# Performance work log

Hardware: AMD Instinct MI355X
Metric: run time of the kernel (lower is better)

Reference implementation:

```python
import jax, jax.numpy as jnp
import numpy as np

I, O, R = 64, 64, 896          # input / output / regulatory protein counts
N = I + O + R                  # total GRN size
WARMUP = 25                    # warmup_count


def setup_inputs() -> dict:
    key = jax.random.key(0)
    k1, k2, k3, k4 = jax.random.split(key, 4)
    return {
        "inputs": jax.random.uniform(k1, (16384, I), dtype=jnp.float32),
        "identifiers": jax.random.uniform(k2, (N,), dtype=jnp.float32),
        "enhancers": jax.random.uniform(k3, (N,), dtype=jnp.float32),
        "inhibitors": jax.random.uniform(k4, (N,), dtype=jnp.float32),
        "beta": jnp.full((1,), 2.0, dtype=jnp.float32),
        "delta": jnp.full((1,), 1.0, dtype=jnp.float32),
    }


def _signatures(identifiers, enhancers, inhibitors, beta):
    # sig[j, i] = exp(-beta * |tag_j - id_i|): affinity of protein j regulating protein i.
    enh = jnp.exp(-beta * jnp.abs(enhancers[:, None] - identifiers[None, :]))
    inh = jnp.exp(-beta * jnp.abs(inhibitors[:, None] - identifiers[None, :]))
    # output proteins do not regulate others -> zero their rows
    mask = jnp.ones((N,), dtype=enh.dtype).at[I:I + O].set(0.0)[:, None]
    return enh * mask, inh * mask


def _step(conc, sig_diff, delta):
    # conc: [..., N]; sig_diff = enh_sigs - inh_sigs: [N, N]
    dc = (delta / N) * (conc @ sig_diff)
    new = jnp.maximum(conc + dc, 0.0)
    reg = new[..., I:]                                    # outputs + regulatory
    s = jnp.sum(reg, axis=-1, keepdims=True)
    reg = jnp.where(s > 0, reg / s, reg)                  # renormalize
    return jnp.concatenate([conc[..., :I], reg], axis=-1)  # inputs clamped


def reference(inputs, identifiers, enhancers, inhibitors, beta, delta):
    b, d = beta[0], delta[0]
    enh_s, inh_s = _signatures(identifiers, enhancers, inhibitors, b)
    sig_diff = enh_s - inh_s

    # setup(): uniform initial concentrations; warmup(): shared sequential steps
    conc0 = jnp.full((N,), 1.0 / N, dtype=jnp.float32)
    def warm(c, _):
        return _step(c, sig_diff, d), None
    conc, _ = jax.lax.scan(warm, conc0, None, length=WARMUP)

    # per-sample (batched instead of tf.map_fn): set input concs, one step
    B = inputs.shape[0]
    batch_conc = jnp.concatenate(
        [inputs, jnp.broadcast_to(conc[I:], (B, N - I))], axis=-1)
    new = _step(batch_conc, sig_diff, d)
    return new[..., I:I + O]  # output protein concentrations [B, O]
```

## Files before the change

kernel.cpp:

```cpp
#include <hip/hip_runtime.h>
#include <math.h>

#define NJ 960
#define NSRC 896
#define NWARM 25

typedef unsigned long long u64;
typedef unsigned int u32;

#define RK_O   0u
#define CT_O   896u
#define HD_O   1856u
#define WK_F   8192u
#define BASE_F (WK_F + 64u * 960u)

#define TAG_RK 0x524B0001u
#define TAG_CT 0x43540001u
#define TAG_HD 0x48440001u

__device__ __forceinline__ void ast(u64* p, u64 v) {
  __hip_atomic_store(p, v, __ATOMIC_RELAXED, __HIP_MEMORY_SCOPE_AGENT);
}
__device__ __forceinline__ u64 ald(const u64* p) {
  return __hip_atomic_load(p, __ATOMIC_RELAXED, __HIP_MEMORY_SCOPE_AGENT);
}
__device__ __forceinline__ u32 poll32(const u64* p, u32 tag) {
  u64 v = ald(p);
  while ((u32)(v >> 32) != tag) { __builtin_amdgcn_s_sleep(1); v = ald(p); }
  return (u32)v;
}

__global__ __launch_bounds__(256) void front_k(const float* __restrict__ ident,
                                               const float* __restrict__ enh,
                                               const float* __restrict__ inh,
                                               const float* __restrict__ beta,
                                               const float* __restrict__ delta,
                                               void* __restrict__ wsv) {
  u64* RK = (u64*)wsv + RK_O;
  u64* CT = (u64*)wsv + CT_O;
  u64* HD = (u64*)wsv + HD_O;
  float* Wk = (float*)wsv + WK_F;
  float* base = (float*)wsv + BASE_F;

  const int tid = threadIdx.x;
  const float bb = beta[0];
  const float dN = delta[0] / 1024.0f;

  if (blockIdx.x > 0) {
    const int g = (blockIdx.x - 1) * 256 + tid;
    const int c8 = g & 7;
    if (g < NSRC * 8) {
      int m = g >> 3;
      float myE = enh[128 + m], myI = inh[128 + m];
      int re = 0, ri = 0;
      for (int i = 112 * c8; i < 112 * c8 + 112; ++i) {
        float ev = enh[128 + i], iv = inh[128 + i];
        re += (ev < myE || (ev == myE && i < m)) ? 1 : 0;
        ri += (iv < myI || (iv == myI && i < m)) ? 1 : 0;
      }
      int p = re | (ri << 16);
      p += __shfl_xor(p, 1); p += __shfl_xor(p, 2); p += __shfl_xor(p, 4);
      if (c8 == 0) ast(&RK[m], ((u64)TAG_RK << 32) | (u32)p);
    }
    {
      int j = g >> 3;
      float cj = ident[64 + j];
      int ce = 0, ci = 0;
      for (int i = 112 * c8; i < 112 * c8 + 112; ++i) {
        ce += (enh[128 + i] <= cj) ? 1 : 0;
        ci += (inh[128 + i] <= cj) ? 1 : 0;
      }
      int p = ce | (ci << 16);
      p += __shfl_xor(p, 1); p += __shfl_xor(p, 2); p += __shfl_xor(p, 4);
      if (c8 == 0) ast(&CT[j], ((u64)TAG_CT << 32) | (u32)p);
    }
    {
      int j = g >> 3;
      float cj = ident[64 + j];
      float h = 0.0f;
      for (int k = 8 * c8; k < 8 * c8 + 8; ++k)
        h += expf(-bb * fabsf(enh[k] - cj)) - expf(-bb * fabsf(inh[k] - cj));
      h += __shfl_xor(h, 1); h += __shfl_xor(h, 2); h += __shfl_xor(h, 4);
      if (c8 == 0)
        ast(&HD[j], ((u64)TAG_HD << 32) |
                    (u64)__float_as_uint(dN * h * (1.0f / 1024.0f)));
    }
    {
      int k = g / 120;
      int jb = (g % 120) * 8;
      float ek = enh[k], ik = inh[k];
      #pragma unroll
      for (int u = 0; u < 8; ++u) {
        float cj = ident[64 + jb + u];
        Wk[(size_t)k * NJ + jb + u] =
            dN * (expf(-bb * fabsf(ek - cj)) - expf(-bb * fabsf(ik - cj)));
      }
    }
    return;
  }

  __shared__ float yl[NJ];
  __shared__ float2 scanE[1024];
  __shared__ float2 scanI[1024];
  __shared__ float4 wtot[4];
  __shared__ float ssw[4];

  const int lane = tid & 63, wvid = tid >> 6;

  int rE[4], rI[4];
  if (tid < 224) {
    #pragma unroll
    for (int s = 0; s < 4; ++s) {
      u32 v = poll32(&RK[4 * tid + s], TAG_RK);
      rE[s] = v & 0xFFFF; rI[s] = v >> 16;
    }
  }
  int cE[4], cI[4];
  float hd[4], fm[4], fp[4];
  if (tid < 240) {
    #pragma unroll
    for (int c = 0; c < 4; ++c) {
      u32 v = poll32(&CT[4 * tid + c], TAG_CT);
      cE[c] = v & 0xFFFF; cI[c] = v >> 16;
      hd[c] = __uint_as_float(poll32(&HD[4 * tid + c], TAG_HD));
      float cj = ident[64 + 4 * tid + c];
      fm[c] = expf(-bb * cj); fp[c] = expf(bb * cj);
    }
  }
  float EP[4], EN[4], IP[4], IN2[4];
  if (tid < 224) {
    #pragma unroll
    for (int s = 0; s < 4; ++s) {
      float e = enh[128 + 4 * tid + s], i2 = inh[128 + 4 * tid + s];
      EP[s] = expf(bb * e);  EN[s] = expf(-bb * e);
      IP[s] = expf(bb * i2); IN2[s] = expf(-bb * i2);
    }
  }
  float y_own[4] = {1.0f / 1024.0f, 1.0f / 1024.0f, 1.0f / 1024.0f, 1.0f / 1024.0f};
  if (tid < 240) {
    #pragma unroll
    for (int c = 0; c < 4; ++c) yl[4 * tid + c] = 1.0f / 1024.0f;
  }
  __syncthreads();

  for (int t = 0; t <= NWARM; ++t) {
    if (tid == 0) {
      scanE[0] = make_float2(0.f, 0.f);
      scanI[0] = make_float2(0.f, 0.f);
    }
    if (tid >= 224) {
      #pragma unroll
      for (int c = 0; c < 4; ++c) {
        int p = 4 * tid + c;
        if (p > NSRC) {
          scanE[p] = make_float2(0.f, 0.f);
          scanI[p] = make_float2(0.f, 0.f);
        }
      }
    }
    if (tid < 224) {
      #pragma unroll
      for (int s = 0; s < 4; ++s) {
        float ym = yl[64 + 4 * tid + s];
        scanE[rE[s] + 1] = make_float2(ym * EP[s], ym * EN[s]);
        scanI[rI[s] + 1] = make_float2(ym * IP[s], ym * IN2[s]);
      }
    }
    __syncthreads();

    float2 e0 = scanE[4 * tid], e1 = scanE[4 * tid + 1],
           e2 = scanE[4 * tid + 2], e3 = scanE[4 * tid + 3];
    float2 i0 = scanI[4 * tid], i1 = scanI[4 * tid + 1],
           i2v = scanI[4 * tid + 2], i3 = scanI[4 * tid + 3];
    e1.x += e0.x; e1.y += e0.y; e2.x += e1.x; e2.y += e1.y; e3.x += e2.x; e3.y += e2.y;
    i1.x += i0.x; i1.y += i0.y; i2v.x += i1.x; i2v.y += i1.y; i3.x += i2v.x; i3.y += i2v.y;
    float4 tot = make_float4(e3.x, e3.y, i3.x, i3.y);
    float4 inc = tot;
    #pragma unroll
    for (int off = 1; off < 64; off <<= 1) {
      float ox = __shfl_up(inc.x, off, 64);
      float oy = __shfl_up(inc.y, off, 64);
      float oz = __shfl_up(inc.z, off, 64);
      float ow = __shfl_up(inc.w, off, 64);
      if (lane >= off) { inc.x += ox; inc.y += oy; inc.z += oz; inc.w += ow; }
    }
    if (lane == 63) wtot[wvid] = inc;
    __syncthreads();
    float4 exc = make_float4(inc.x - tot.x, inc.y - tot.y,
                             inc.z - tot.z, inc.w - tot.w);
    #pragma unroll
    for (int w = 0; w < 3; ++w)
      if (w < wvid) {
        float4 p = wtot[w];
        exc.x += p.x; exc.y += p.y; exc.z += p.z; exc.w += p.w;
      }
    e0.x += exc.x; e0.y += exc.y; e1.x += exc.x; e1.y += exc.y;
    e2.x += exc.x; e2.y += exc.y; e3.x += exc.x; e3.y += exc.y;
    i0.x += exc.z; i0.y += exc.w; i1.x += exc.z; i1.y += exc.w;
    i2v.x += exc.z; i2v.y += exc.w; i3.x += exc.z; i3.y += exc.w;
    scanE[4 * tid] = e0; scanE[4 * tid + 1] = e1;
    scanE[4 * tid + 2] = e2; scanE[4 * tid + 3] = e3;
    scanI[4 * tid] = i0; scanI[4 * tid + 1] = i1;
    scanI[4 * tid + 2] = i2v; scanI[4 * tid + 3] = i3;
    __syncthreads();

    float nv[4] = {0.f, 0.f, 0.f, 0.f};
    float psum = 0.0f;
    if (tid < 240) {
      float2 TE = scanE[NSRC], TI = scanI[NSRC];
      #pragma unroll
      for (int c = 0; c < 4; ++c) {
        float2 AE = scanE[cE[c]], AI = scanI[cI[c]];
        float dot = fm[c] * AE.x + fp[c] * (TE.y - AE.y)
                  - fm[c] * AI.x - fp[c] * (TI.y - AI.y);
        float pre = y_own[c] + dN * dot;
        if (t < NWARM) {
          nv[c] = fmaxf(pre + hd[c], 0.0f);
          psum += nv[c];
        } else {
          base[4 * tid + c] = pre;
        }
      }
    }
    if (t < NWARM) {
      #pragma unroll
      for (int off = 32; off >= 1; off >>= 1) psum += __shfl_xor(psum, off);
      if (lane == 0) ssw[wvid] = psum;
      __syncthreads();
      float s = ssw[0] + ssw[1] + ssw[2] + ssw[3];
      float inv = (s > 0.0f) ? 1.0f / s : 1.0f;
      if (tid < 240) {
        #pragma unroll
        for (int c = 0; c < 4; ++c) {
          y_own[c] = nv[c] * inv;
          yl[4 * tid + c] = y_own[c];
        }
      }
    }
    __syncthreads();
  }
}

__global__ __launch_bounds__(512) void batch_t(const float* __restrict__ inp,
                                               const float* __restrict__ ws,
                                               float* __restrict__ out) {
  __shared__ float At[64][66];
  __shared__ float Wl[16][516];
  __shared__ float bch[512];

  const int tid = threadIdx.x;
  const int colg = tid & 63;
  const int rowg = tid >> 6;
  const size_t rowbase = (size_t)blockIdx.x * 64;
  const float* __restrict__ Wk = ws + WK_F;
  const float* __restrict__ base = ws + BASE_F;

  #pragma unroll
  for (int i = 0; i < 2; ++i) {
    int fi = tid + i * 512;
    int r = fi >> 4, c4 = (fi & 15) * 4;
    float4 f4 = *(const float4*)(inp + (rowbase + r) * 64 + c4);
    At[c4 + 0][r] = f4.x; At[c4 + 1][r] = f4.y;
    At[c4 + 2][r] = f4.z; At[c4 + 3][r] = f4.w;
  }

  float rs[8];
  #pragma unroll
  for (int r = 0; r < 8; ++r) rs[r] = 0.0f;
  float acc[8][8];

  #pragma unroll 1
  for (int ch = 0; ch < 2; ++ch) {
    const int c0 = ch ? 0 : 512;
    #pragma unroll
    for (int r = 0; r < 8; ++r)
      #pragma unroll
      for (int c = 0; c < 8; ++c) acc[r][c] = 0.0f;

    __syncthreads();
    {
      int j = c0 + tid;
      bch[tid] = (j < 960) ? base[j] : -1.0e30f;
    }

    #pragma unroll 1
    for (int s = 0; s < 4; ++s) {
      __syncthreads();
      #pragma unroll
      for (int i = 0; i < 4; ++i) {
        int fi = tid + i * 512;
        int kk = fi >> 7;
        int c4 = (fi & 127) * 4;
        int j = c0 + c4;
        float4 v = make_float4(0.f, 0.f, 0.f, 0.f);
        if (j < 960)
          v = *(const float4*)(Wk + (size_t)(16 * s + kk) * NJ + j);
        *(float4*)&Wl[kk][c4] = v;
      }
      __syncthreads();

      #pragma unroll
      for (int kk = 0; kk < 16; ++kk) {
        float4 a0 = *(const float4*)&At[16 * s + kk][rowg * 8];
        float4 a1 = *(const float4*)&At[16 * s + kk][rowg * 8 + 4];
        float4 w0 = *(const float4*)&Wl[kk][colg * 8];
        float4 w1 = *(const float4*)&Wl[kk][colg * 8 + 4];
        float a[8] = {a0.x, a0.y, a0.z, a0.w, a1.x, a1.y, a1.z, a1.w};
        float w[8] = {w0.x, w0.y, w0.z, w0.w, w1.x, w1.y, w1.z, w1.w};
        #pragma unroll
        for (int r = 0; r < 8; ++r)
          #pragma unroll
          for (int c = 0; c < 8; ++c)
            acc[r][c] = fmaf(a[r], w[c], acc[r][c]);
      }
    }

    #pragma unroll
    for (int c = 0; c < 8; ++c) {
      float bv = bch[colg * 8 + c];
      #pragma unroll
      for (int r = 0; r < 8; ++r)
        rs[r] += fmaxf(acc[r][c] + bv, 0.0f);
    }
  }

  #pragma unroll
  for (int r = 0; r < 8; ++r) {
    float v = rs[r];
    #pragma unroll
    for (int off = 32; off >= 1; off >>= 1) v += __shfl_xor(v, off);
    rs[r] = v;
  }

  if (colg < 8) {
    #pragma unroll
    for (int r = 0; r < 8; ++r) {
      float inv = (rs[r] > 0.0f) ? 1.0f / rs[r] : 1.0f;
      float* op = out + (rowbase + rowg * 8 + r) * 64 + colg * 8;
      float4 o;
      o.x = fmaxf(acc[r][0] + bch[colg * 8 + 0], 0.0f) * inv;
      o.y = fmaxf(acc[r][1] + bch[colg * 8 + 1], 0.0f) * inv;
      o.z = fmaxf(acc[r][2] + bch[colg * 8 + 2], 0.0f) * inv;
      o.w = fmaxf(acc[r][3] + bch[colg * 8 + 3], 0.0f) * inv;
      *(float4*)op = o;
      o.x = fmaxf(acc[r][4] + bch[colg * 8 + 4], 0.0f) * inv;
      o.y = fmaxf(acc[r][5] + bch[colg * 8 + 5], 0.0f) * inv;
      o.z = fmaxf(acc[r][6] + bch[colg * 8 + 6], 0.0f) * inv;
      o.w = fmaxf(acc[r][7] + bch[colg * 8 + 7], 0.0f) * inv;
      *(float4*)(op + 4) = o;
    }
  }
}

extern "C" void kernel_launch(void* const* d_in, const int* in_sizes, int n_in,
                              void* d_out, int out_size, void* d_ws, size_t ws_size,
                              hipStream_t stream) {
  const float* inp   = (const float*)d_in[0];
  const float* ident = (const float*)d_in[1];
  const float* enh   = (const float*)d_in[2];
  const float* inh   = (const float*)d_in[3];
  const float* beta  = (const float*)d_in[4];
  const float* delta = (const float*)d_in[5];

  hipLaunchKernelGGL(front_k, dim3(31), dim3(256), 0, stream,
                     ident, enh, inh, beta, delta, d_ws);
  hipLaunchKernelGGL(batch_t, dim3(256), dim3(512), 0, stream,
                     inp, (const float*)d_ws, (float*)d_out);
}
```

Before: 158.6 us.

## Fuse warmup and batch GEMM into one persistent kernel with flag sync

Merges the two launches into a single grid. Block 0 runs the sequential warmup scan and publishes the bias through tagged atomic flags, blocks 1-30 also compute the rank/count tables, and the batch blocks compute their GEMM concurrently. The batch blocks now build the weight matrix on the fly from precomputed exponentials instead of reading a global Wk, and only wait on the done flag before the ReLU/normalise epilogue. This hides the serial warmup latency behind the batch GEMM and removes a launch, at the cost of spin-waiting, a dependence on block 0 getting scheduled, and a 256-thread, 32-row tile with more registers per thread.

Result: slower. 283.7 us (+78.9%).

```diff
diff --git a/kernel.cpp b/kernel.cpp
--- a/kernel.cpp
+++ b/kernel.cpp
@@ -8,15 +8,17 @@
 typedef unsigned long long u64;
 typedef unsigned int u32;
 
-#define RK_O   0u
-#define CT_O   896u
-#define HD_O   1856u
-#define WK_F   8192u
-#define BASE_F (WK_F + 64u * 960u)
+#define RK_O 0u
+#define CT_O 896u
+#define HD_O 1856u
+#define BS_O 2816u
+#define DN_O 3776u
 
 #define TAG_RK 0x524B0001u
 #define TAG_CT 0x43540001u
 #define TAG_HD 0x48440001u
+#define TAG_BS 0x42530001u
+#define TAG_DN 0x444E0001u
 
 __device__ __forceinline__ void ast(u64* p, u64 v) {
   __hip_atomic_store(p, v, __ATOMIC_RELAXED, __HIP_MEMORY_SCOPE_AGENT);
@@ -30,24 +32,181 @@
   return (u32)v;
 }
 
-__global__ __launch_bounds__(256) void front_k(const float* __restrict__ ident,
-                                               const float* __restrict__ enh,
-                                               const float* __restrict__ inh,
-                                               const float* __restrict__ beta,
-                                               const float* __restrict__ delta,
-                                               void* __restrict__ wsv) {
+struct ScanSm {
+  float yl[NJ];
+  float2 scanE[1024];
+  float2 scanI[1024];
+  float4 wtot[4];
+  float ssw[4];
+};
+struct BatSm {
+  float At[64][36];
+  float Wl[16][512];
+  float bchl[NJ];
+  float4 Ek4[64];
+  float2 Ei2[64];
+};
+
+__global__ __launch_bounds__(256, 3) void grn_all(
+    const float* __restrict__ inp, const float* __restrict__ ident,
+    const float* __restrict__ enh, const float* __restrict__ inh,
+    const float* __restrict__ beta, const float* __restrict__ delta,
+    void* __restrict__ wsv, float* __restrict__ out) {
+  __shared__ __align__(16) char smraw[(sizeof(BatSm) > sizeof(ScanSm))
+                                          ? sizeof(BatSm) : sizeof(ScanSm)];
   u64* RK = (u64*)wsv + RK_O;
   u64* CT = (u64*)wsv + CT_O;
   u64* HD = (u64*)wsv + HD_O;
-  float* Wk = (float*)wsv + WK_F;
-  float* base = (float*)wsv + BASE_F;
+  u64* BS = (u64*)wsv + BS_O;
+  u64* DN = (u64*)wsv + DN_O;
 
   const int tid = threadIdx.x;
   const float bb = beta[0];
   const float dN = delta[0] / 1024.0f;
 
-  if (blockIdx.x > 0) {
-    const int g = (blockIdx.x - 1) * 256 + tid;
+  if (blockIdx.x == 0) {
+    ScanSm& S = *(ScanSm*)smraw;
+    const int lane = tid & 63, wvid = tid >> 6;
+
+    int rE[4], rI[4];
+    if (tid < 224) {
+      #pragma unroll
+      for (int s = 0; s < 4; ++s) {
+        u32 v = poll32(&RK[4 * tid + s], TAG_RK);
+        rE[s] = v & 0xFFFF; rI[s] = v >> 16;
+      }
+    }
+    int cE[4], cI[4];
+    float hd[4], fm[4], fp[4];
+    if (tid < 240) {
+      #pragma unroll
+      for (int c = 0; c < 4; ++c) {
+        u32 v = poll32(&CT[4 * tid + c], TAG_CT);
+        cE[c] = v & 0xFFFF; cI[c] = v >> 16;
+        hd[c] = __uint_as_float(poll32(&HD[4 * tid + c], TAG_HD));
+        float cj = ident[64 + 4 * tid + c];
+        fm[c] = expf(-bb * cj); fp[c] = expf(bb * cj);
+      }
+    }
+    float EP[4], EN[4], IP[4], IN2[4];
+    if (tid < 224) {
+      #pragma unroll
+      for (int s = 0; s < 4; ++s) {
+        float e = enh[128 + 4 * tid + s], i2 = inh[128 + 4 * tid + s];
+        EP[s] = expf(bb * e);  EN[s] = expf(-bb * e);
+        IP[s] = expf(bb * i2); IN2[s] = expf(-bb * i2);
+      }
+    }
+    float y_own[4] = {1.0f / 1024.0f, 1.0f / 1024.0f, 1.0f / 1024.0f, 1.0f / 1024.0f};
+    if (tid < 240) {
+      #pragma unroll
+      for (int c = 0; c < 4; ++c) S.yl[4 * tid + c] = 1.0f / 1024.0f;
+    }
+    __syncthreads();
+
+    for (int t = 0; t <= NWARM; ++t) {
+      if (tid == 0) {
+        S.scanE[0] = make_float2(0.f, 0.f);
+        S.scanI[0] = make_float2(0.f, 0.f);
+      }
+      if (tid >= 224) {
+        #pragma unroll
+        for (int c = 0; c < 4; ++c) {
+          int p = 4 * tid + c;
+          if (p > NSRC) {
+            S.scanE[p] = make_float2(0.f, 0.f);
+            S.scanI[p] = make_float2(0.f, 0.f);
+          }
+        }
+      }
+      if (tid < 224) {
+        #pragma unroll
+        for (int s = 0; s < 4; ++s) {
+          float ym = S.yl[64 + 4 * tid + s];
+          S.scanE[rE[s] + 1] = make_float2(ym * EP[s], ym * EN[s]);
+          S.scanI[rI[s] + 1] = make_float2(ym * IP[s], ym * IN2[s]);
+        }
+      }
+      __syncthreads();
+
+      float2 e0 = S.scanE[4 * tid], e1 = S.scanE[4 * tid + 1],
+             e2 = S.scanE[4 * tid + 2], e3 = S.scanE[4 * tid + 3];
+      float2 i0 = S.scanI[4 * tid], i1 = S.scanI[4 * tid + 1],
+             i2v = S.scanI[4 * tid + 2], i3 = S.scanI[4 * tid + 3];
+      e1.x += e0.x; e1.y += e0.y; e2.x += e1.x; e2.y += e1.y; e3.x += e2.x; e3.y += e2.y;
+      i1.x += i0.x; i1.y += i0.y; i2v.x += i1.x; i2v.y += i1.y; i3.x += i2v.x; i3.y += i2v.y;
+      float4 tot = make_float4(e3.x, e3.y, i3.x, i3.y);
+      float4 inc = tot;
+      #pragma unroll
+      for (int off = 1; off < 64; off <<= 1) {
+        float ox = __shfl_up(inc.x, off, 64);
+        float oy = __shfl_up(inc.y, off, 64);
+        float oz = __shfl_up(inc.z, off, 64);
+        float ow = __shfl_up(inc.w, off, 64);
+        if (lane >= off) { inc.x += ox; inc.y += oy; inc.z += oz; inc.w += ow; }
+      }
+      if (lane == 63) S.wtot[wvid] = inc;
+      __syncthreads();
+      float4 exc = make_float4(inc.x - tot.x, inc.y - tot.y,
+                               inc.z - tot.z, inc.w - tot.w);
+      #pragma unroll
+      for (int w = 0; w < 3; ++w)
+        if (w < wvid) {
+          float4 p = S.wtot[w];
+          exc.x += p.x; exc.y += p.y; exc.z += p.z; exc.w += p.w;
+        }
+      e0.x += exc.x; e0.y += exc.y; e1.x += exc.x; e1.y += exc.y;
+      e2.x += exc.x; e2.y += exc.y; e3.x += exc.x; e3.y += exc.y;
+      i0.x += exc.z; i0.y += exc.w; i1.x += exc.z; i1.y += exc.w;
+      i2v.x += exc.z; i2v.y += exc.w; i3.x += exc.z; i3.y += exc.w;
+      S.scanE[4 * tid] = e0; S.scanE[4 * tid + 1] = e1;
+      S.scanE[4 * tid + 2] = e2; S.scanE[4 * tid + 3] = e3;
+      S.scanI[4 * tid] = i0; S.scanI[4 * tid + 1] = i1;
+      S.scanI[4 * tid + 2] = i2v; S.scanI[4 * tid + 3] = i3;
+      __syncthreads();
+
+      float nv[4] = {0.f, 0.f, 0.f, 0.f};
+      float psum = 0.0f;
+      if (tid < 240) {
+        float2 TE = S.scanE[NSRC], TI = S.scanI[NSRC];
+        #pragma unroll
+        for (int c = 0; c < 4; ++c) {
+          float2 AE = S.scanE[cE[c]], AI = S.scanI[cI[c]];
+          float dot = fm[c] * AE.x + fp[c] * (TE.y - AE.y)
+                    - fm[c] * AI.x - fp[c] * (TI.y - AI.y);
+          float pre = y_own[c] + dN * dot;
+          if (t < NWARM) {
+            nv[c] = fmaxf(pre + hd[c], 0.0f);
+            psum += nv[c];
+          } else {
+            ast(&BS[4 * tid + c],
+                ((u64)TAG_BS << 32) | (u64)__float_as_uint(pre));
+          }
+        }
+      }
+      if (t < NWARM) {
+        #pragma unroll
+        for (int off = 32; off >= 1; off >>= 1) psum += __shfl_xor(psum, off);
+        if (lane == 0) S.ssw[wvid] = psum;
+        __syncthreads();
+        float s2 = S.ssw[0] + S.ssw[1] + S.ssw[2] + S.ssw[3];
+        float inv = (s2 > 0.0f) ? 1.0f / s2 : 1.0f;
+        if (tid < 240) {
+          #pragma unroll
+          for (int c = 0; c < 4; ++c) {
+            y_own[c] = nv[c] * inv;
+            S.yl[4 * tid + c] = y_own[c];
+          }
+        }
+      }
+      __syncthreads();
+    }
+    if (tid == 0) ast(DN, ((u64)TAG_DN << 32) | 1u);
+    return;
+  }
+
+  if (blockIdx.x <= 30) {
+    const int g = (int)(blockIdx.x - 1) * 256 + tid;
     const int c8 = g & 7;
     if (g < NSRC * 8) {
       int m = g >> 3;
@@ -85,245 +244,117 @@
         ast(&HD[j], ((u64)TAG_HD << 32) |
                     (u64)__float_as_uint(dN * h * (1.0f / 1024.0f)));
     }
-    {
-      int k = g / 120;
-      int jb = (g % 120) * 8;
-      float ek = enh[k], ik = inh[k];
-      #pragma unroll
-      for (int u = 0; u < 8; ++u) {
-        float cj = ident[64 + jb + u];
-        Wk[(size_t)k * NJ + jb + u] =
-            dN * (expf(-bb * fabsf(ek - cj)) - expf(-bb * fabsf(ik - cj)));
-      }
-    }
-    return;
-  }
-
-  __shared__ float yl[NJ];
-  __shared__ float2 scanE[1024];
-  __shared__ float2 scanI[1024];
-  __shared__ float4 wtot[4];
-  __shared__ float ssw[4];
-
-  const int lane = tid & 63, wvid = tid >> 6;
-
-  int rE[4], rI[4];
-  if (tid < 224) {
-    #pragma unroll
-    for (int s = 0; s < 4; ++s) {
-      u32 v = poll32(&RK[4 * tid + s], TAG_RK);
-      rE[s] = v & 0xFFFF; rI[s] = v >> 16;
-    }
-  }
-  int cE[4], cI[4];
-  float hd[4], fm[4], fp[4];
-  if (tid < 240) {
-    #pragma unroll
-    for (int c = 0; c < 4; ++c) {
-      u32 v = poll32(&CT[4 * tid + c], TAG_CT);
-      cE[c] = v & 0xFFFF; cI[c] = v >> 16;
-      hd[c] = __uint_as_float(poll32(&HD[4 * tid + c], TAG_HD));
-      float cj = ident[64 + 4 * tid + c];
-      fm[c] = expf(-bb * cj); fp[c] = expf(bb * cj);
-    }
-  }
-  float EP[4], EN[4], IP[4], IN2[4];
-  if (tid < 224) {
-    #pragma unroll
-    for (int s = 0; s < 4; ++s) {
-      float e = enh[128 + 4 * tid + s], i2 = inh[128 + 4 * tid + s];
-      EP[s] = expf(bb * e);  EN[s] = expf(-bb * e);
-      IP[s] = expf(bb * i2); IN2[s] = expf(-bb * i2);
-    }
-  }
-  float y_own[4] = {1.0f / 1024.0f, 1.0f / 1024.0f, 1.0f / 1024.0f, 1.0f / 1024.0f};
-  if (tid < 240) {
-    #pragma unroll
-    for (int c = 0; c < 4; ++c) yl[4 * tid + c] = 1.0f / 1024.0f;
-  }
-  __syncthreads();
-
-  for (int t = 0; t <= NWARM; ++t) {
-    if (tid == 0) {
-      scanE[0] = make_float2(0.f, 0.f);
-      scanI[0] = make_float2(0.f, 0.f);
-    }
-    if (tid >= 224) {
-      #pragma unroll
-      for (int c = 0; c < 4; ++c) {
-        int p = 4 * tid + c;
-        if (p > NSRC) {
-          scanE[p] = make_float2(0.f, 0.f);
-          scanI[p] = make_float2(0.f, 0.f);
-        }
-      }
-    }
-    if (tid < 224) {
-      #pragma unroll
-      for (int s = 0; s < 4; ++s) {
-        float ym = yl[64 + 4 * tid + s];
-        scanE[rE[s] + 1] = make_float2(ym * EP[s], ym * EN[s]);
-        scanI[rI[s] + 1] = make_float2(ym * IP[s], ym * IN2[s]);
-      }
-    }
-    __syncthreads();
-
-    float2 e0 = scanE[4 * tid], e1 = scanE[4 * tid + 1],
-           e2 = scanE[4 * tid + 2], e3 = scanE[4 * tid + 3];
-    float2 i0 = scanI[4 * tid], i1 = scanI[4 * tid + 1],
-           i2v = scanI[4 * tid + 2], i3 = scanI[4 * tid + 3];
-    e1.x += e0.x; e1.y += e0.y; e2.x += e1.x; e2.y += e1.y; e3.x += e2.x; e3.y += e2.y;
-    i1.x += i0.x; i1.y += i0.y; i2v.x += i1.x; i2v.y += i1.y; i3.x += i2v.x; i3.y += i2v.y;
-    float4 tot = make_float4(e3.x, e3.y, i3.x, i3.y);
-    float4 inc = tot;
-    #pragma unroll
-    for (int off = 1; off < 64; off <<= 1) {
-      float ox = __shfl_up(inc.x, off, 64);
-      float oy = __shfl_up(inc.y, off, 64);
-      float oz = __shfl_up(inc.z, off, 64);
-      float ow = __shfl_up(inc.w, off, 64);
-      if (lane >= off) { inc.x += ox; inc.y += oy; inc.z += oz; inc.w += ow; }
-    }
-    if (lane == 63) wtot[wvid] = inc;
-    __syncthreads();
-    float4 exc = make_float4(inc.x - tot.x, inc.y - tot.y,
-                             inc.z - tot.z, inc.w - tot.w);
-    #pragma unroll
-    for (int w = 0; w < 3; ++w)
-      if (w < wvid) {
-        float4 p = wtot[w];
-        exc.x += p.x; exc.y += p.y; exc.z += p.z; exc.w += p.w;
-      }
-    e0.x += exc.x; e0.y += exc.y; e1.x += exc.x; e1.y += exc.y;
-    e2.x += exc.x; e2.y += exc.y; e3.x += exc.x; e3.y += exc.y;
-    i0.x += exc.z; i0.y += exc.w; i1.x += exc.z; i1.y += exc.w;
-    i2v.x += exc.z; i2v.y += exc.w; i3.x += exc.z; i3.y += exc.w;
-    scanE[4 * tid] = e0; scanE[4 * tid + 1] = e1;
-    scanE[4 * tid + 2] = e2; scanE[4 * tid + 3] = e3;
-    scanI[4 * tid] = i0; scanI[4 * tid + 1] = i1;
-    scanI[4 * tid + 2] = i2v; scanI[4 * tid + 3] = i3;
-    __syncthreads();
-
-    float nv[4] = {0.f, 0.f, 0.f, 0.f};
-    float psum = 0.0f;
-    if (tid < 240) {
-      float2 TE = scanE[NSRC], TI = scanI[NSRC];
-      #pragma unroll
-      for (int c = 0; c < 4; ++c) {
-        float2 AE = scanE[cE[c]], AI = scanI[cI[c]];
-        float dot = fm[c] * AE.x + fp[c] * (TE.y - AE.y)
-                  - fm[c] * AI.x - fp[c] * (TI.y - AI.y);
-        float pre = y_own[c] + dN * dot;
-        if (t < NWARM) {
-          nv[c] = fmaxf(pre + hd[c], 0.0f);
-          psum += nv[c];
-        } else {
-          base[4 * tid + c] = pre;
-        }
-      }
-    }
-    if (t < NWARM) {
-      #pragma unroll
-      for (int off = 32; off >= 1; off >>= 1) psum += __shfl_xor(psum, off);
-      if (lane == 0) ssw[wvid] = psum;
-      __syncthreads();
-      float s = ssw[0] + ssw[1] + ssw[2] + ssw[3];
-      float inv = (s > 0.0f) ? 1.0f / s : 1.0f;
-      if (tid < 240) {
-        #pragma unroll
-        for (int c = 0; c < 4; ++c) {
-          y_own[c] = nv[c] * inv;
-          yl[4 * tid + c] = y_own[c];
-        }
-      }
-    }
-    __syncthreads();
-  }
-}
-
-__global__ __launch_bounds__(512) void batch_t(const float* __restrict__ inp,
-                                               const float* __restrict__ ws,
-                                               float* __restrict__ out) {
-  __shared__ float At[64][66];
-  __shared__ float Wl[16][516];
-  __shared__ float bch[512];
-
-  const int tid = threadIdx.x;
+  }
+
+  BatSm& Bm = *(BatSm*)smraw;
   const int colg = tid & 63;
   const int rowg = tid >> 6;
-  const size_t rowbase = (size_t)blockIdx.x * 64;
-  const float* __restrict__ Wk = ws + WK_F;
-  const float* __restrict__ base = ws + BASE_F;
+  const size_t rowbase = (size_t)(blockIdx.x - 1) * 32;
 
   #pragma unroll
   for (int i = 0; i < 2; ++i) {
-    int fi = tid + i * 512;
+    int fi = tid + i * 256;
     int r = fi >> 4, c4 = (fi & 15) * 4;
     float4 f4 = *(const float4*)(inp + (rowbase + r) * 64 + c4);
-    At[c4 + 0][r] = f4.x; At[c4 + 1][r] = f4.y;
-    At[c4 + 2][r] = f4.z; At[c4 + 3][r] = f4.w;
-  }
-
-  float rs[8];
-  #pragma unroll
-  for (int r = 0; r < 8; ++r) rs[r] = 0.0f;
-  float acc[8][8];
-
-  #pragma unroll 1
+    Bm.At[c4 + 0][r] = f4.x; Bm.At[c4 + 1][r] = f4.y;
+    Bm.At[c4 + 2][r] = f4.z; Bm.At[c4 + 3][r] = f4.w;
+  }
+  if (tid < 64) {
+    float e = enh[tid], iv = inh[tid];
+    Bm.Ek4[tid] = make_float4(expf(bb * e), expf(-bb * e),
+                              expf(bb * iv), expf(-bb * iv));
+    Bm.Ei2[tid] = make_float2(e, iv);
+  }
+
+  float acc[2][8][8];
+  #pragma unroll
+  for (int r = 0; r < 8; ++r)
+    #pragma unroll
+    for (int c = 0; c < 8; ++c) { acc[0][r][c] = 0.0f; acc[1][r][c] = 0.0f; }
+
+  #pragma unroll
   for (int ch = 0; ch < 2; ++ch) {
     const int c0 = ch ? 0 : 512;
-    #pragma unroll
-    for (int r = 0; r < 8; ++r)
-      #pragma unroll
-      for (int c = 0; c < 8; ++c) acc[r][c] = 0.0f;
-
-    __syncthreads();
-    {
-      int j = c0 + tid;
-      bch[tid] = (j < 960) ? base[j] : -1.0e30f;
-    }
+    const int jA = c0 + tid;
+    const int jB = c0 + 256 + tid;
+    const bool okB = (jB < NJ);
+    float cjA = ident[64 + jA];
+    float cjB = okB ? ident[64 + jB] : 0.0f;
+    float fpA = expf(bb * cjA), fmA = expf(-bb * cjA);
+    float fpB = expf(bb * cjB), fmB = expf(-bb * cjB);
 
     #pragma unroll 1
     for (int s = 0; s < 4; ++s) {
       __syncthreads();
       #pragma unroll
-      for (int i = 0; i < 4; ++i) {
-        int fi = tid + i * 512;
-        int kk = fi >> 7;
-        int c4 = (fi & 127) * 4;
-        int j = c0 + c4;
-        float4 v = make_float4(0.f, 0.f, 0.f, 0.f);
-        if (j < 960)
-          v = *(const float4*)(Wk + (size_t)(16 * s + kk) * NJ + j);
-        *(float4*)&Wl[kk][c4] = v;
-      }
-      __syncthreads();
-
+      for (int e = 0; e < 16; ++e) {
+        int k = 16 * s + e;
+        float4 E = Bm.Ek4[k];
+        float2 ei = Bm.Ei2[k];
+        float wA = dN * (((ei.x >= cjA) ? E.y * fpA : E.x * fmA)
+                       - ((ei.y >= cjA) ? E.w * fpA : E.z * fmA));
+        Bm.Wl[e][tid] = wA;
+        float wB = 0.0f;
+        if (okB)
+          wB = dN * (((ei.x >= cjB) ? E.y * fpB : E.x * fmB)
+                   - ((ei.y >= cjB) ? E.w * fpB : E.z * fmB));
+        Bm.Wl[e][tid + 256] = wB;
+      }
+      __syncthreads();
       #pragma unroll
       for (int kk = 0; kk < 16; ++kk) {
-        float4 a0 = *(const float4*)&At[16 * s + kk][rowg * 8];
-        float4 a1 = *(const float4*)&At[16 * s + kk][rowg * 8 + 4];
-        float4 w0 = *(const float4*)&Wl[kk][colg * 8];
-        float4 w1 = *(const float4*)&Wl[kk][colg * 8 + 4];
+        float4 a0 = *(const float4*)&Bm.At[16 * s + kk][rowg * 8];
+        float4 a1 = *(const float4*)&Bm.At[16 * s + kk][rowg * 8 + 4];
+        float4 w0 = *(const float4*)&Bm.Wl[kk][colg * 4];
+        float4 w1 = *(const float4*)&Bm.Wl[kk][256 + colg * 4];
         float a[8] = {a0.x, a0.y, a0.z, a0.w, a1.x, a1.y, a1.z, a1.w};
         float w[8] = {w0.x, w0.y, w0.z, w0.w, w1.x, w1.y, w1.z, w1.w};
-        #pragma unroll
-        for (int r = 0; r < 8; ++r)
+        if (ch == 0) {
           #pragma unroll
-          for (int c = 0; c < 8; ++c)
-            acc[r][c] = fmaf(a[r], w[c], acc[r][c]);
-      }
-    }
-
+          for (int r = 0; r < 8; ++r)
+            #pragma unroll
+            for (int c = 0; c < 8; ++c)
+              acc[0][r][c] = fmaf(a[r], w[c], acc[0][r][c]);
+        } else {
+          #pragma unroll
+          for (int r = 0; r < 8; ++r)
+            #pragma unroll
+            for (int c = 0; c < 8; ++c)
+              acc[1][r][c] = fmaf(a[r], w[c], acc[1][r][c]);
+        }
+      }
+    }
+  }
+
+  if (tid == 0) {
+    u64 v = ald(DN);
+    while ((u32)(v >> 32) != TAG_DN) { __builtin_amdgcn_s_sleep(32); v = ald(DN); }
+  }
+  __syncthreads();
+  if (tid < 120) {
     #pragma unroll
     for (int c = 0; c < 8; ++c) {
-      float bv = bch[colg * 8 + c];
-      #pragma unroll
-      for (int r = 0; r < 8; ++r)
-        rs[r] += fmaxf(acc[r][c] + bv, 0.0f);
-    }
-  }
-
+      int j = 8 * tid + c;
+      Bm.bchl[j] = __uint_as_float(poll32(&BS[j], TAG_BS));
+    }
+  }
+  __syncthreads();
+
+  float rs[8];
+  #pragma unroll
+  for (int r = 0; r < 8; ++r) rs[r] = 0.0f;
+  #pragma unroll
+  for (int c = 0; c < 8; ++c) {
+    int cl = (c < 4) ? (colg * 4 + c) : (256 + colg * 4 + (c - 4));
+    int col0 = 512 + cl;
+    float bv0 = (col0 < NJ) ? Bm.bchl[col0] : -1.0e30f;
+    float bv1 = Bm.bchl[cl];
+    #pragma unroll
+    for (int r = 0; r < 8; ++r) {
+      rs[r] += fmaxf(acc[0][r][c] + bv0, 0.0f);
+      rs[r] += fmaxf(acc[1][r][c] + bv1, 0.0f);
+    }
+  }
   #pragma unroll
   for (int r = 0; r < 8; ++r) {
     float v = rs[r];
@@ -331,23 +362,17 @@
     for (int off = 32; off >= 1; off >>= 1) v += __shfl_xor(v, off);
     rs[r] = v;
   }
-
-  if (colg < 8) {
+  if (colg < 16) {
     #pragma unroll
     for (int r = 0; r < 8; ++r) {
       float inv = (rs[r] > 0.0f) ? 1.0f / rs[r] : 1.0f;
-      float* op = out + (rowbase + rowg * 8 + r) * 64 + colg * 8;
+      float* op = out + (rowbase + rowg * 8 + r) * 64 + colg * 4;
       float4 o;
-      o.x = fmaxf(acc[r][0] + bch[colg * 8 + 0], 0.0f) * inv;
-      o.y = fmaxf(acc[r][1] + bch[colg * 8 + 1], 0.0f) * inv;
-      o.z = fmaxf(acc[r][2] + bch[colg * 8 + 2], 0.0f) * inv;
-      o.w = fmaxf(acc[r][3] + bch[colg * 8 + 3], 0.0f) * inv;
+      o.x = fmaxf(acc[1][r][0] + Bm.bchl[colg * 4 + 0], 0.0f) * inv;
+      o.y = fmaxf(acc[1][r][1] + Bm.bchl[colg * 4 + 1], 0.0f) * inv;
+      o.z = fmaxf(acc[1][r][2] + Bm.bchl[colg * 4 + 2], 0.0f) * inv;
+      o.w = fmaxf(acc[1][r][3] + Bm.bchl[colg * 4 + 3], 0.0f) * inv;
       *(float4*)op = o;
-      o.x = fmaxf(acc[r][4] + bch[colg * 8 + 4], 0.0f) * inv;
-      o.y = fmaxf(acc[r][5] + bch[colg * 8 + 5], 0.0f) * inv;
-      o.z = fmaxf(acc[r][6] + bch[colg * 8 + 6], 0.0f) * inv;
-      o.w = fmaxf(acc[r][7] + bch[colg * 8 + 7], 0.0f) * inv;
-      *(float4*)(op + 4) = o;
     }
   }
 }
@@ -362,8 +387,6 @@
   const float* beta  = (const float*)d_in[4];
   const float* delta = (const float*)d_in[5];
 
-  hipLaunchKernelGGL(front_k, dim3(31), dim3(256), 0, stream,
-                     ident, enh, inh, beta, delta, d_ws);
-  hipLaunchKernelGGL(batch_t, dim3(256), dim3(512), 0, stream,
-                     inp, (const float*)d_ws, (float*)d_out);
-}
+  hipLaunchKernelGGL(grn_all, dim3(513), dim3(256), 0, stream,
+                     inp, ident, enh, inh, beta, delta, d_ws, (float*)d_out);
+}
```

## Compute input-row weight matrix on the fly inside batch kernel via factored exponentials

Applied to the files above, without the earlier changes.

Each batch block now builds the 64x960 input-to-target weight tile in shared memory, instead of front_k writing it to the workspace for batch_k to read back. It uses the identity exp(-b|x-c|) = exp(±bx)·exp(∓bc), with per-source and per-column exponentials precomputed. The column mapping changes to interleaved 4-wide groups so that Wl writes are conflict-free and the whole bias row is staged once. This removes global Wk traffic and front_k's expf work. The cost is redundant weight computation in every block and a possible loss of accuracy for large beta*value products.

Result: no change. 160.8 us (+1.4%).

```diff
diff --git a/kernel.cpp b/kernel.cpp
--- a/kernel.cpp
+++ b/kernel.cpp
@@ -8,11 +8,10 @@
 typedef unsigned long long u64;
 typedef unsigned int u32;
 
-#define RK_O   0u
-#define CT_O   896u
-#define HD_O   1856u
-#define WK_F   8192u
-#define BASE_F (WK_F + 64u * 960u)
+#define RK_O 0u
+#define CT_O 896u
+#define HD_O 1856u
+#define BASE_F 8192u
 
 #define TAG_RK 0x524B0001u
 #define TAG_CT 0x43540001u
@@ -39,7 +38,6 @@
   u64* RK = (u64*)wsv + RK_O;
   u64* CT = (u64*)wsv + CT_O;
   u64* HD = (u64*)wsv + HD_O;
-  float* Wk = (float*)wsv + WK_F;
   float* base = (float*)wsv + BASE_F;
 
   const int tid = threadIdx.x;
@@ -47,7 +45,7 @@
   const float dN = delta[0] / 1024.0f;
 
   if (blockIdx.x > 0) {
-    const int g = (blockIdx.x - 1) * 256 + tid;
+    const int g = (int)(blockIdx.x - 1) * 256 + tid;
     const int c8 = g & 7;
     if (g < NSRC * 8) {
       int m = g >> 3;
@@ -84,17 +82,6 @@
       if (c8 == 0)
         ast(&HD[j], ((u64)TAG_HD << 32) |
                     (u64)__float_as_uint(dN * h * (1.0f / 1024.0f)));
-    }
-    {
-      int k = g / 120;
-      int jb = (g % 120) * 8;
-      float ek = enh[k], ik = inh[k];
-      #pragma unroll
-      for (int u = 0; u < 8; ++u) {
-        float cj = ident[64 + jb + u];
-        Wk[(size_t)k * NJ + jb + u] =
-            dN * (expf(-bb * fabsf(ek - cj)) - expf(-bb * fabsf(ik - cj)));
-      }
     }
     return;
   }
@@ -241,19 +228,26 @@
   }
 }
 
-__global__ __launch_bounds__(512) void batch_t(const float* __restrict__ inp,
+__global__ __launch_bounds__(512) void batch_k(const float* __restrict__ inp,
+                                               const float* __restrict__ ident,
+                                               const float* __restrict__ enh,
+                                               const float* __restrict__ inh,
+                                               const float* __restrict__ beta,
+                                               const float* __restrict__ delta,
                                                const float* __restrict__ ws,
                                                float* __restrict__ out) {
   __shared__ float At[64][66];
-  __shared__ float Wl[16][516];
-  __shared__ float bch[512];
+  __shared__ float Wl[16][512];
+  __shared__ float bch[NJ];
+  __shared__ float4 Ek4[64];
+  __shared__ float2 Ei2[64];
 
   const int tid = threadIdx.x;
   const int colg = tid & 63;
   const int rowg = tid >> 6;
   const size_t rowbase = (size_t)blockIdx.x * 64;
-  const float* __restrict__ Wk = ws + WK_F;
-  const float* __restrict__ base = ws + BASE_F;
+  const float bb = beta[0];
+  const float dN = delta[0] / 1024.0f;
 
   #pragma unroll
   for (int i = 0; i < 2; ++i) {
@@ -263,61 +257,71 @@
     At[c4 + 0][r] = f4.x; At[c4 + 1][r] = f4.y;
     At[c4 + 2][r] = f4.z; At[c4 + 3][r] = f4.w;
   }
-
+  if (tid < 64) {
+    float e = enh[tid], iv = inh[tid];
+    Ek4[tid] = make_float4(expf(bb * e), expf(-bb * e),
+                           expf(bb * iv), expf(-bb * iv));
+    Ei2[tid] = make_float2(e, iv);
+  }
+  if (tid < 240) {
+    float4 b4 = *(const float4*)(ws + BASE_F + 4 * tid);
+    bch[4 * tid + 0] = b4.x; bch[4 * tid + 1] = b4.y;
+    bch[4 * tid + 2] = b4.z; bch[4 * tid + 3] = b4.w;
+  }
+
+  float acc[8][8];
   float rs[8];
   #pragma unroll
   for (int r = 0; r < 8; ++r) rs[r] = 0.0f;
-  float acc[8][8];
 
   #pragma unroll 1
   for (int ch = 0; ch < 2; ++ch) {
     const int c0 = ch ? 0 : 512;
+    const bool ok = (c0 + tid) < NJ;
+    const float cj = ok ? ident[64 + c0 + tid] : 0.0f;
+    const float fpc = expf(bb * cj), fmc = expf(-bb * cj);
+
     #pragma unroll
     for (int r = 0; r < 8; ++r)
       #pragma unroll
       for (int c = 0; c < 8; ++c) acc[r][c] = 0.0f;
-
-    __syncthreads();
-    {
-      int j = c0 + tid;
-      bch[tid] = (j < 960) ? base[j] : -1.0e30f;
-    }
 
     #pragma unroll 1
     for (int s = 0; s < 4; ++s) {
       __syncthreads();
-      #pragma unroll
-      for (int i = 0; i < 4; ++i) {
-        int fi = tid + i * 512;
-        int kk = fi >> 7;
-        int c4 = (fi & 127) * 4;
-        int j = c0 + c4;
-        float4 v = make_float4(0.f, 0.f, 0.f, 0.f);
-        if (j < 960)
-          v = *(const float4*)(Wk + (size_t)(16 * s + kk) * NJ + j);
-        *(float4*)&Wl[kk][c4] = v;
+      #pragma unroll 4
+      for (int e = 0; e < 16; ++e) {
+        int k = 16 * s + e;
+        float4 E = Ek4[k];
+        float2 ei = Ei2[k];
+        float w = 0.0f;
+        if (ok)
+          w = dN * (((ei.x >= cj) ? E.y * fpc : E.x * fmc)
+                  - ((ei.y >= cj) ? E.w * fpc : E.z * fmc));
+        Wl[e][tid] = w;
       }
       __syncthreads();
-
       #pragma unroll
       for (int kk = 0; kk < 16; ++kk) {
         float4 a0 = *(const float4*)&At[16 * s + kk][rowg * 8];
         float4 a1 = *(const float4*)&At[16 * s + kk][rowg * 8 + 4];
-        float4 w0 = *(const float4*)&Wl[kk][colg * 8];
-        float4 w1 = *(const float4*)&Wl[kk][colg * 8 + 4];
-        float a[8] = {a0.x, a0.y, a0.z, a0.w, a1.x, a1.y, a1.z, a1.w};
-        float w[8] = {w0.x, w0.y, w0.z, w0.w, w1.x, w1.y, w1.z, w1.w};
+        float4 w0 = *(const float4*)&Wl[kk][colg * 4];
+        float4 w1 = *(const float4*)&Wl[kk][256 + colg * 4];
+        float a_[8] = {a0.x, a0.y, a0.z, a0.w, a1.x, a1.y, a1.z, a1.w};
+        float w_[8] = {w0.x, w0.y, w0.z, w0.w, w1.x, w1.y, w1.z, w1.w};
         #pragma unroll
         for (int r = 0; r < 8; ++r)
           #pragma unroll
           for (int c = 0; c < 8; ++c)
-            acc[r][c] = fmaf(a[r], w[c], acc[r][c]);
+            acc[r][c] = fmaf(a_[r], w_[c], acc[r][c]);
       }
     }
 
     #pragma unroll
     for (int c = 0; c < 8; ++c) {
-      float bv = bch[colg * 8 + c];
+      int cl = (c < 4) ? (colg * 4 + c) : (256 + colg * 4 + (c - 4));
+      int j = c0 + cl;
+      float bv = (j < NJ) ? bch[j] : -1.0e30f;
       #pragma unroll
       for (int r = 0; r < 8; ++r)
         rs[r] += fmaxf(acc[r][c] + bv, 0.0f);
@@ -331,23 +335,17 @@
     for (int off = 32; off >= 1; off >>= 1) v += __shfl_xor(v, off);
     rs[r] = v;
   }
-
-  if (colg < 8) {
+  if (colg < 16) {
     #pragma unroll
     for (int r = 0; r < 8; ++r) {
       float inv = (rs[r] > 0.0f) ? 1.0f / rs[r] : 1.0f;
-      float* op = out + (rowbase + rowg * 8 + r) * 64 + colg * 8;
+      float* op = out + (rowbase + rowg * 8 + r) * 64 + colg * 4;
       float4 o;
-      o.x = fmaxf(acc[r][0] + bch[colg * 8 + 0], 0.0f) * inv;
-      o.y = fmaxf(acc[r][1] + bch[colg * 8 + 1], 0.0f) * inv;
-      o.z = fmaxf(acc[r][2] + bch[colg * 8 + 2], 0.0f) * inv;
-      o.w = fmaxf(acc[r][3] + bch[colg * 8 + 3], 0.0f) * inv;
+      o.x = fmaxf(acc[r][0] + bch[colg * 4 + 0], 0.0f) * inv;
+      o.y = fmaxf(acc[r][1] + bch[colg * 4 + 1], 0.0f) * inv;
+      o.z = fmaxf(acc[r][2] + bch[colg * 4 + 2], 0.0f) * inv;
+      o.w = fmaxf(acc[r][3] + bch[colg * 4 + 3], 0.0f) * inv;
       *(float4*)op = o;
-      o.x = fmaxf(acc[r][4] + bch[colg * 8 + 4], 0.0f) * inv;
-      o.y = fmaxf(acc[r][5] + bch[colg * 8 + 5], 0.0f) * inv;
-      o.z = fmaxf(acc[r][6] + bch[colg * 8 + 6], 0.0f) * inv;
-      o.w = fmaxf(acc[r][7] + bch[colg * 8 + 7], 0.0f) * inv;
-      *(float4*)(op + 4) = o;
     }
   }
 }
@@ -364,6 +362,7 @@
 
   hipLaunchKernelGGL(front_k, dim3(31), dim3(256), 0, stream,
                      ident, enh, inh, beta, delta, d_ws);
-  hipLaunchKernelGGL(batch_t, dim3(256), dim3(512), 0, stream,
-                     inp, (const float*)d_ws, (float*)d_out);
-}
+  hipLaunchKernelGGL(batch_k, dim3(256), dim3(512), 0, stream,
+                     inp, ident, enh, inh, beta, delta,
+                     (const float*)d_ws, (float*)d_out);
+}
```
